# Kernel tuning notes

Measured on AMD Instinct MI355X. Metric: run time of the kernel, lower is better.

Reference implementation:

```python
import math
import jax, jax.numpy as jnp
import numpy as np

B, TQ, TK = 16, 2048, 1024
D_DEC, D_ENC, D_ATT = 256, 256, 128
WINDOW_SIZE = 3


def setup_inputs() -> dict:
    key = jax.random.key(0)
    ks = jax.random.split(key, 11)
    s = 0.02
    return {
        "query": jax.random.normal(ks[0], (B, TQ, D_DEC), jnp.float32),
        "keys": jax.random.normal(ks[1], (B, TK, D_ENC), jnp.float32),
        "values": jax.random.normal(ks[2], (B, TK, D_ENC), jnp.float32),
        "Wq": jax.random.normal(ks[3], (D_ATT, D_DEC), jnp.float32) * s,
        "bq": jax.random.normal(ks[4], (D_ATT,), jnp.float32) * s,
        "Wk": jax.random.normal(ks[5], (D_ATT, D_ENC), jnp.float32) * s,
        "bk": jax.random.normal(ks[6], (D_ATT,), jnp.float32) * s,
        "Wv": jax.random.normal(ks[7], (D_ATT, D_ENC), jnp.float32) * s,
        "bv": jax.random.normal(ks[8], (D_ATT,), jnp.float32) * s,
        "Wo": jax.random.normal(ks[9], (D_DEC, D_ATT), jnp.float32) * s,
        "bo": jax.random.normal(ks[10], (D_DEC,), jnp.float32) * s,
        "prev_max_attention_idx": 100,
    }


def reference(query, keys, values, Wq, bq, Wk, bk, Wv, bv, Wo, bo,
              prev_max_attention_idx):
    residual = query
    q = query @ Wq.T + bq            # [B, Tq, A]
    k = keys @ Wk.T + bk             # [B, Tk, A]
    v = values @ Wv.T + bv           # [B, Tk, A]
    scores = jnp.einsum('bqa,bka->bqk', q, k)  # [B, Tq, Tk]
    Tk = scores.shape[-1]
    col = jnp.arange(Tk)
    # mask [:prev] if prev > 0, and [prev + window :] if in range
    masked = (col < prev_max_attention_idx) | (col >= prev_max_attention_idx + WINDOW_SIZE)
    scores = jnp.where(masked[None, None, :], -jnp.inf, scores)
    attn = jax.nn.softmax(scores, axis=-1)
    attn_scores = attn
    # dropout_prob = 0.0 -> identity
    ctx = jnp.einsum('bqk,bka->bqa', attn, v)
    s = v.shape[1]
    ctx = ctx * (s * math.sqrt(1.0 / s))  # == sqrt(Tk)
    out = (ctx @ Wo.T + bo + residual) * math.sqrt(0.5)
    return (out, attn_scores)
```

## Files before the change

### kernel.cpp

```cpp
#include <hip/hip_runtime.h>
#include <math.h>

#define BATCH 16
#define TQL   2048
#define TKL   1024
#define DDEC  256
#define DENC  256
#define DATT  128
#define WIN   3

#define WS_KQ 0
#define WS_VO (48*DDEC)
#define WS_KB (2*48*DDEC)

#define NZBLK 2048

__global__ __launch_bounds__(256) void pre_and_zero(
    const float* __restrict__ keys, const float* __restrict__ values,
    const float* __restrict__ Wk, const float* __restrict__ bk,
    const float* __restrict__ Wv, const float* __restrict__ bv,
    const float* __restrict__ Wq, const float* __restrict__ bq,
    const float* __restrict__ Wo, const int* __restrict__ pidx,
    float* __restrict__ ws, float* __restrict__ attn)
{
    const int t = threadIdx.x;

    if (blockIdx.x >= 48) {
        const int zb = blockIdx.x - 48;
        float4* p = (float4*)attn + (size_t)zb * 4096;
        const float4 z4 = make_float4(0.0f, 0.0f, 0.0f, 0.0f);
        #pragma unroll
        for (int i = 0; i < 16; ++i) p[i * 256 + t] = z4;
        return;
    }

    const int blk = blockIdx.x;
    const int b = blk / WIN, j = blk % WIN;
    const int prev = pidx[0];
    const int col = prev + j;
    const bool valid = (col >= 0) && (col < TKL);

    __shared__ float ksh[DENC];
    __shared__ float vsh[DENC];
    __shared__ float kwsh[DATT];
    __shared__ float vwsh[DATT];

    {
        size_t base = ((size_t)b * TKL + (valid ? col : 0)) * DENC + t;
        ksh[t] = valid ? keys[base]   : 0.0f;
        vsh[t] = valid ? values[base] : 0.0f;
    }
    __syncthreads();

    if (t < DATT) {
        const float4* wrow = (const float4*)(Wk + (size_t)t * DENC);
        float acc = 0.0f;
        #pragma unroll 8
        for (int k4 = 0; k4 < DENC / 4; ++k4) {
            float4 w = wrow[k4];
            acc += w.x * ksh[k4*4+0] + w.y * ksh[k4*4+1]
                 + w.z * ksh[k4*4+2] + w.w * ksh[k4*4+3];
        }
        kwsh[t] = acc + bk[t];
    } else {
        const int c = t - DATT;
        const float4* wrow = (const float4*)(Wv + (size_t)c * DENC);
        float acc = 0.0f;
        #pragma unroll 8
        for (int k4 = 0; k4 < DENC / 4; ++k4) {
            float4 w = wrow[k4];
            acc += w.x * vsh[k4*4+0] + w.y * vsh[k4*4+1]
                 + w.z * vsh[k4*4+2] + w.w * vsh[k4*4+3];
        }
        vwsh[c] = acc + bv[c];
    }
    __syncthreads();

    float accq = 0.0f, acco = 0.0f;
    const float4* worow = (const float4*)(Wo + (size_t)t * DATT);
    #pragma unroll 4
    for (int c4 = 0; c4 < DATT / 4; ++c4) {
        float4 w = worow[c4];
        acco += w.x * vwsh[c4*4+0] + w.y * vwsh[c4*4+1]
              + w.z * vwsh[c4*4+2] + w.w * vwsh[c4*4+3];
        accq += kwsh[c4*4+0] * Wq[(size_t)(c4*4+0) * DDEC + t]
              + kwsh[c4*4+1] * Wq[(size_t)(c4*4+1) * DDEC + t]
              + kwsh[c4*4+2] * Wq[(size_t)(c4*4+2) * DDEC + t]
              + kwsh[c4*4+3] * Wq[(size_t)(c4*4+3) * DDEC + t];
    }
    ws[WS_KQ + blk * DDEC + t] = accq;
    ws[WS_VO + blk * DDEC + t] = acco;

    if (t < 64) {
        float pb = bq[t] * kwsh[t] + bq[t + 64] * kwsh[t + 64];
        #pragma unroll
        for (int off = 32; off > 0; off >>= 1) pb += __shfl_xor(pb, off, 64);
        if (t == 0) ws[WS_KB + blk] = pb;
    }
}

__device__ __forceinline__ float winval(int ww, float w0, float w1, float w2) {
    float v = (ww == 0) ? w0 : ((ww == 1) ? w1 : ((ww == 2) ? w2 : 0.0f));
    return (ww >= 0 && ww < WIN) ? v : 0.0f;
}

__device__ __forceinline__ void process_row(
    int row, int sub, int prev, int f0, int f1,
    const float4 q0, const float4 q1, const float4 q2, const float4 q3,
    const float* kqsh, const float* vosh, const float* bosh, const float* kbsh,
    float* __restrict__ out, float* __restrict__ attn)
{
    const float4* kq4 = (const float4*)kqsh;
    const float4* vo4 = (const float4*)vosh;
    const float4* bo4 = (const float4*)bosh;

    float p0, p1, p2;
    {
        float4 k0, k1, k2;
        k0 = kq4[ 0 + sub]; k1 = kq4[ 64 + sub]; k2 = kq4[128 + sub];
        p0  = q0.x*k0.x + q0.y*k0.y + q0.z*k0.z + q0.w*k0.w;
        p1  = q0.x*k1.x + q0.y*k1.y + q0.z*k1.z + q0.w*k1.w;
        p2  = q0.x*k2.x + q0.y*k2.y + q0.z*k2.z + q0.w*k2.w;
        k0 = kq4[16 + sub]; k1 = kq4[ 80 + sub]; k2 = kq4[144 + sub];
        p0 += q1.x*k0.x + q1.y*k0.y + q1.z*k0.z + q1.w*k0.w;
        p1 += q1.x*k1.x + q1.y*k1.y + q1.z*k1.z + q1.w*k1.w;
        p2 += q1.x*k2.x + q1.y*k2.y + q1.z*k2.z + q1.w*k2.w;
        k0 = kq4[32 + sub]; k1 = kq4[ 96 + sub]; k2 = kq4[160 + sub];
        p0 += q2.x*k0.x + q2.y*k0.y + q2.z*k0.z + q2.w*k0.w;
        p1 += q2.x*k1.x + q2.y*k1.y + q2.z*k1.z + q2.w*k1.w;
        p2 += q2.x*k2.x + q2.y*k2.y + q2.z*k2.z + q2.w*k2.w;
        k0 = kq4[48 + sub]; k1 = kq4[112 + sub]; k2 = kq4[176 + sub];
        p0 += q3.x*k0.x + q3.y*k0.y + q3.z*k0.z + q3.w*k0.w;
        p1 += q3.x*k1.x + q3.y*k1.y + q3.z*k1.z + q3.w*k1.w;
        p2 += q3.x*k2.x + q3.y*k2.y + q3.z*k2.z + q3.w*k2.w;
    }
    #pragma unroll
    for (int off = 8; off > 0; off >>= 1) {
        p0 += __shfl_xor(p0, off, 64);
        p1 += __shfl_xor(p1, off, 64);
        p2 += __shfl_xor(p2, off, 64);
    }

    float s0 = p0 + kbsh[0];
    float s1 = p1 + kbsh[1];
    float s2 = p2 + kbsh[2];

    const bool v0 = (prev + 0 >= 0) && (prev + 0 < TKL);
    const bool v1 = (prev + 1 >= 0) && (prev + 1 < TKL);
    const bool v2 = (prev + 2 >= 0) && (prev + 2 < TKL);
    const float NEG = -3.0e38f;
    if (!v0) s0 = NEG;
    if (!v1) s1 = NEG;
    if (!v2) s2 = NEG;

    const float m  = fmaxf(s0, fmaxf(s1, s2));
    const float e0 = v0 ? __expf(s0 - m) : 0.0f;
    const float e1 = v1 ? __expf(s1 - m) : 0.0f;
    const float e2 = v2 ? __expf(s2 - m) : 0.0f;
    const float inv = 1.0f / (e0 + e1 + e2);
    const float w0 = e0 * inv, w1 = e1 * inv, w2 = e2 * inv;

    const float CTX_SCALE = 32.0f;
    const float RSQ2 = 0.70710678118654752f;

    float4* orow = (float4*)(out + (size_t)row * DDEC);
    #pragma unroll
    for (int k = 0; k < 4; ++k) {
        const float4 x0 = vo4[k * 16 + sub];
        const float4 x1 = vo4[k * 16 + 64 + sub];
        const float4 x2 = vo4[k * 16 + 128 + sub];
        const float4 bb = bo4[k * 16 + sub];
        const float4 qq = (k == 0) ? q0 : (k == 1) ? q1 : (k == 2) ? q2 : q3;
        float4 o;
        o.x = (CTX_SCALE * (w0*x0.x + w1*x1.x + w2*x2.x) + bb.x + qq.x) * RSQ2;
        o.y = (CTX_SCALE * (w0*x0.y + w1*x1.y + w2*x2.y) + bb.y + qq.y) * RSQ2;
        o.z = (CTX_SCALE * (w0*x0.z + w1*x1.z + w2*x2.z) + bb.z + qq.z) * RSQ2;
        o.w = (CTX_SCALE * (w0*x0.w + w1*x1.w + w2*x2.w) + bb.w + qq.w) * RSQ2;
        orow[k * 16 + sub] = o;
    }

    if (f0 >= 0) {
        float4* arow = (float4*)(attn + (size_t)row * TKL);
        if ((f0 & 15) == sub) {
            const int c0 = f0 * 4;
            float4 pz;
            pz.x = winval(c0 + 0 - prev, w0, w1, w2);
            pz.y = winval(c0 + 1 - prev, w0, w1, w2);
            pz.z = winval(c0 + 2 - prev, w0, w1, w2);
            pz.w = winval(c0 + 3 - prev, w0, w1, w2);
            arow[f0] = pz;
        }
        if (f1 != f0 && (f1 & 15) == sub) {
            const int c0 = f1 * 4;
            float4 pz;
            pz.x = winval(c0 + 0 - prev, w0, w1, w2);
            pz.y = winval(c0 + 1 - prev, w0, w1, w2);
            pz.z = winval(c0 + 2 - prev, w0, w1, w2);
            pz.w = winval(c0 + 3 - prev, w0, w1, w2);
            arow[f1] = pz;
        }
    }
}

__global__ __launch_bounds__(256) void attn_out(
    const float* __restrict__ query, const float* __restrict__ bo,
    const int* __restrict__ pidx, const float* __restrict__ ws,
    float* __restrict__ out, float* __restrict__ attn)
{
    const int t   = threadIdx.x;
    const int G   = t >> 4;
    const int sub = t & 15;
    const int blk = blockIdx.x;
    const int b   = blk >> 6;
    const int base = b * WIN;
    const int prev = pidx[0];

    const int rowA = blk * 32 + G;
    const int rowB = rowA + 16;

    const float4* qA = (const float4*)query + (size_t)rowA * 64;
    const float4* qB = (const float4*)query + (size_t)rowB * 64;
    const float4 a0 = qA[ 0 + sub], a1 = qA[16 + sub],
                 a2 = qA[32 + sub], a3 = qA[48 + sub];
    const float4 b0 = qB[ 0 + sub], b1 = qB[16 + sub],
                 b2 = qB[32 + sub], b3 = qB[48 + sub];

    __shared__ float kqsh[3 * DDEC];
    __shared__ float vosh[3 * DDEC];
    __shared__ float bosh[DDEC];
    __shared__ float kbsh[WIN];
    #pragma unroll
    for (int j = 0; j < 3; ++j) {
        kqsh[j * DDEC + t] = ws[WS_KQ + (base + j) * DDEC + t];
        vosh[j * DDEC + t] = ws[WS_VO + (base + j) * DDEC + t];
    }
    bosh[t] = bo[t];
    if (t < WIN) kbsh[t] = ws[WS_KB + base + t];
    __syncthreads();

    int lo = prev < 0 ? 0 : prev;
    int hi = prev + (WIN - 1) > TKL - 1 ? TKL - 1 : prev + (WIN - 1);
    int f0 = -1, f1 = -1;
    if (lo <= hi) { f0 = lo >> 2; f1 = hi >> 2; }

    process_row(rowA, sub, prev, f0, f1, a0, a1, a2, a3,
                kqsh, vosh, bosh, kbsh, out, attn);
    process_row(rowB, sub, prev, f0, f1, b0, b1, b2, b3,
                kqsh, vosh, bosh, kbsh, out, attn);
}

extern "C" void kernel_launch(void* const* d_in, const int* in_sizes, int n_in,
                              void* d_out, int out_size, void* d_ws, size_t ws_size,
                              hipStream_t stream)
{
    const float* query  = (const float*)d_in[0];
    const float* keys   = (const float*)d_in[1];
    const float* values = (const float*)d_in[2];
    const float* Wq     = (const float*)d_in[3];
    const float* bq     = (const float*)d_in[4];
    const float* Wk     = (const float*)d_in[5];
    const float* bk     = (const float*)d_in[6];
    const float* Wv     = (const float*)d_in[7];
    const float* bv     = (const float*)d_in[8];
    const float* Wo     = (const float*)d_in[9];
    const float* bo     = (const float*)d_in[10];
    const int*   pidx   = (const int*)d_in[11];

    float* ws   = (float*)d_ws;
    float* out  = (float*)d_out;
    float* attn = out + (size_t)BATCH * TQL * DDEC;

    pre_and_zero<<<48 + NZBLK, 256, 0, stream>>>(keys, values, Wk, bk, Wv, bv,
                                                 Wq, bq, Wo, pidx, ws, attn);
    attn_out<<<BATCH * TQL / 32, 256, 0, stream>>>(query, bo, pidx, ws, out, attn);
}
```

Measured before the change: 41.26 us.

## Split attention zero-fill across both kernels to overlap with compute

```diff
diff --git a/kernel.cpp b/kernel.cpp
--- a/kernel.cpp
+++ b/kernel.cpp
@@ -13,9 +13,17 @@
 #define WS_VO (48*DDEC)
 #define WS_KB (2*48*DDEC)
 
-#define NZBLK 2048
-
-__global__ __launch_bounds__(256) void pre_and_zero(
+#define NFILL1 512
+#define NFILL2 1536
+
+__device__ __forceinline__ void window_f4(int prev, int* f0, int* f1) {
+    int lo = prev < 0 ? 0 : prev;
+    int hi = prev + (WIN - 1) > TKL - 1 ? TKL - 1 : prev + (WIN - 1);
+    *f0 = -1; *f1 = -1;
+    if (lo <= hi) { *f0 = lo >> 2; *f1 = hi >> 2; }
+}
+
+__global__ __launch_bounds__(256) void pre_and_fill0(
     const float* __restrict__ keys, const float* __restrict__ values,
     const float* __restrict__ Wk, const float* __restrict__ bk,
     const float* __restrict__ Wv, const float* __restrict__ bv,
@@ -26,11 +34,15 @@
     const int t = threadIdx.x;
 
     if (blockIdx.x >= 48) {
+        int f0, f1;
+        window_f4(pidx[0], &f0, &f1);
         const int zb = blockIdx.x - 48;
-        float4* p = (float4*)attn + (size_t)zb * 4096;
+        float4* arow = (float4*)attn + (size_t)zb * 4096;
         const float4 z4 = make_float4(0.0f, 0.0f, 0.0f, 0.0f);
+        const bool wr = (t != f0) && (t != f1);
         #pragma unroll
-        for (int i = 0; i < 16; ++i) p[i * 256 + t] = z4;
+        for (int rr = 0; rr < 16; ++rr)
+            if (wr) arow[rr * 256 + t] = z4;
         return;
     }
 
@@ -202,18 +214,34 @@
     }
 }
 
-__global__ __launch_bounds__(256) void attn_out(
+__global__ __launch_bounds__(256) void fill_and_compute(
     const float* __restrict__ query, const float* __restrict__ bo,
     const int* __restrict__ pidx, const float* __restrict__ ws,
     float* __restrict__ out, float* __restrict__ attn)
 {
-    const int t   = threadIdx.x;
+    const int t    = threadIdx.x;
+    const int role = blockIdx.x % 5;
+    const int grp  = blockIdx.x / 5;
+    const int prev = pidx[0];
+    int f0, f1;
+    window_f4(prev, &f0, &f1);
+
+    if (role >= 2) {
+        const int fid = grp * 3 + (role - 2);
+        float4* arow = (float4*)attn + (size_t)(NFILL1 + fid) * 4096;
+        const float4 z4 = make_float4(0.0f, 0.0f, 0.0f, 0.0f);
+        const bool wr = (t != f0) && (t != f1);
+        #pragma unroll
+        for (int rr = 0; rr < 16; ++rr)
+            if (wr) arow[rr * 256 + t] = z4;
+        return;
+    }
+
+    const int blk = grp * 2 + role;
     const int G   = t >> 4;
     const int sub = t & 15;
-    const int blk = blockIdx.x;
     const int b   = blk >> 6;
     const int base = b * WIN;
-    const int prev = pidx[0];
 
     const int rowA = blk * 32 + G;
     const int rowB = rowA + 16;
@@ -237,11 +265,6 @@
     bosh[t] = bo[t];
     if (t < WIN) kbsh[t] = ws[WS_KB + base + t];
     __syncthreads();
-
-    int lo = prev < 0 ? 0 : prev;
-    int hi = prev + (WIN - 1) > TKL - 1 ? TKL - 1 : prev + (WIN - 1);
-    int f0 = -1, f1 = -1;
-    if (lo <= hi) { f0 = lo >> 2; f1 = hi >> 2; }
 
     process_row(rowA, sub, prev, f0, f1, a0, a1, a2, a3,
                 kqsh, vosh, bosh, kbsh, out, attn);
@@ -270,7 +293,7 @@
     float* out  = (float*)d_out;
     float* attn = out + (size_t)BATCH * TQL * DDEC;
 
-    pre_and_zero<<<48 + NZBLK, 256, 0, stream>>>(keys, values, Wk, bk, Wv, bv,
-                                                 Wq, bq, Wo, pidx, ws, attn);
-    attn_out<<<BATCH * TQL / 32, 256, 0, stream>>>(query, bo, pidx, ws, out, attn);
-}
+    pre_and_fill0<<<48 + NFILL1, 256, 0, stream>>>(keys, values, Wk, bk, Wv, bv,
+                                                   Wq, bq, Wo, pidx, ws, attn);
+    fill_and_compute<<<1024 + NFILL2, 256, 0, stream>>>(query, bo, pidx, ws, out, attn);
+}
```

Result: slower. 46.54 us (+12.8%).
